# Kernel optimization log

Measured on AMD Instinct MI355X. Metric: run time of the kernel, lower is better.

Reference implementation:

```python
import jax, jax.numpy as jnp
import numpy as np

N_EMBD = 2048
N_HEAD = 16
N_HIDDEN = 5632  # find_multiple(int(2*4*2048/3), 256)
EPS = 1e-5
BETA = 1.0


def rmsnorm(x, scale):
    # mean of squares computed in fp32 as in the torch code
    norm = jnp.mean(x.astype(jnp.float32) ** 2, axis=-1, keepdims=True)
    x_normed = x * jax.lax.rsqrt(norm + EPS)
    return (scale * x_normed).astype(x.dtype)


def setup_inputs() -> dict:
    key = jax.random.key(0)
    ks = jax.random.split(key, 9)
    B, T, C = 1, 2048, N_EMBD
    s = lambda k, shape, fan: jax.random.normal(k, shape, jnp.float32) * (1.0 / np.sqrt(fan))
    return {
        "x": jax.random.normal(ks[0], (B, T, C), jnp.float32),
        "alibi": jax.random.normal(ks[1], (N_HEAD, T, T), jnp.float32),
        "w_attn": s(ks[2], (C, 3 * C), C),   # c_attn weight (in, out) layout
        "w_proj": s(ks[3], (C, C), C),
        "w_fc1": s(ks[4], (C, N_HIDDEN), C),
        "w_fc2": s(ks[5], (C, N_HIDDEN), C),
        "w_mlp_proj": s(ks[6], (N_HIDDEN, C), N_HIDDEN),
        "rms1_scale": jnp.ones((C,), jnp.float32),
        "rms2_scale": jnp.ones((C,), jnp.float32),
    }


def attention(x, alibi, w_attn, w_proj):
    B, T, C = x.shape
    hd = C // N_HEAD
    qkv = x @ w_attn  # [B,T,3C]
    q, k, v = jnp.split(qkv, 3, axis=-1)
    q = q.reshape(B, T, N_HEAD, hd).transpose(0, 2, 1, 3)  # [B,H,T,hd]
    k = k.reshape(B, T, N_HEAD, hd).transpose(0, 2, 1, 3)
    v = v.reshape(B, T, N_HEAD, hd).transpose(0, 2, 1, 3)
    scale = 1.0 / np.sqrt(hd)
    scores = jnp.einsum("bhqd,bhkd->bhqk", q, k) * scale + BETA * alibi  # [B,H,T,T]
    causal = jnp.tril(jnp.ones((T, T), bool))
    scores = jnp.where(causal, scores, -jnp.inf)
    attn = jax.nn.softmax(scores, axis=-1)
    y = jnp.einsum("bhqk,bhkd->bhqd", attn, v)
    y = y.transpose(0, 2, 1, 3).reshape(B, T, C)
    return y @ w_proj


def mlp(x, w_fc1, w_fc2, w_mlp_proj):
    return (jax.nn.silu(x @ w_fc1) * (x @ w_fc2)) @ w_mlp_proj


def reference(x, alibi, w_attn, w_proj, w_fc1, w_fc2, w_mlp_proj, rms1_scale, rms2_scale):
    x = x + attention(rmsnorm(x, rms1_scale), alibi, w_attn, w_proj)
    x = x + mlp(rmsnorm(x, rms2_scale), w_fc1, w_fc2, w_mlp_proj)
    return x
```

## Files before the change

kernel.cpp:

```cpp
#include <hip/hip_runtime.h>
#include <stdint.h>

typedef __attribute__((ext_vector_type(4))) float f32x4;
typedef __attribute__((ext_vector_type(8))) __bf16 bf8_t;
typedef __attribute__((ext_vector_type(8))) uint16_t u16x8;

typedef __attribute__((address_space(1))) uint8_t as1_u8;
typedef __attribute__((address_space(3))) uint8_t as3_u8;

__device__ inline void async_copy16(const void* g, void* l) {
  __builtin_amdgcn_global_load_lds((const as1_u8*)g, (as3_u8*)l, 16, 0, 0);
}

__device__ inline uint16_t f2bf(float f) {
  uint32_t u = __builtin_bit_cast(uint32_t, f);
  u = (u + 0x7fff + ((u >> 16) & 1)) >> 16;
  return (uint16_t)u;
}
__device__ inline float bf2f(uint16_t h) {
  uint32_t u = ((uint32_t)h) << 16;
  return __builtin_bit_cast(float, u);
}
__device__ inline int swz(int r) { return (((r & 7) ^ ((r >> 3) & 7)) << 4); }
__device__ inline int vswz(int r) { return ((r & 7) << 4); }

__global__ __launch_bounds__(256) void rmsnorm_kernel(const float* __restrict__ X,
                                                      const float* __restrict__ S,
                                                      uint16_t* __restrict__ O) {
  const int row = blockIdx.x;
  const int tid = threadIdx.x;
  const float* xr = X + (size_t)row * 2048;
  float4 v1 = ((const float4*)xr)[tid * 2];
  float4 v2 = ((const float4*)xr)[tid * 2 + 1];
  float ss = v1.x * v1.x + v1.y * v1.y + v1.z * v1.z + v1.w * v1.w +
             v2.x * v2.x + v2.y * v2.y + v2.z * v2.z + v2.w * v2.w;
  #pragma unroll
  for (int m = 1; m < 64; m <<= 1) ss += __shfl_xor(ss, m);
  __shared__ float wsum[4];
  if ((tid & 63) == 0) wsum[tid >> 6] = ss;
  __syncthreads();
  float tot = wsum[0] + wsum[1] + wsum[2] + wsum[3];
  float inv = rsqrtf(tot * (1.0f / 2048.0f) + 1e-5f);
  const int base = tid * 8;
  const float* sc = S + base;
  float xs[8] = {v1.x, v1.y, v1.z, v1.w, v2.x, v2.y, v2.z, v2.w};
  u16x8 o;
  #pragma unroll
  for (int j = 0; j < 8; j++) o[j] = f2bf(xs[j] * inv * sc[j]);
  *(u16x8*)(O + (size_t)row * 2048 + base) = o;
}

__global__ __launch_bounds__(256) void transpose_conv(const float* __restrict__ W,
                                                      uint16_t* __restrict__ WT,
                                                      int K, int N) {
  __shared__ float tile[64][65];
  const int n0 = blockIdx.x * 64, k0 = blockIdx.y * 64;
  const int tid = threadIdx.x;
  const int lr = tid >> 4;
  const int lc = (tid & 15) * 4;
  #pragma unroll
  for (int i = 0; i < 4; i++) {
    const float4 v = *(const float4*)&W[(size_t)(k0 + lr + i * 16) * N + n0 + lc];
    tile[lr + i * 16][lc] = v.x;
    tile[lr + i * 16][lc + 1] = v.y;
    tile[lr + i * 16][lc + 2] = v.z;
    tile[lr + i * 16][lc + 3] = v.w;
  }
  __syncthreads();
  const int tn = tid >> 3;
  const int tk = (tid & 7) * 8;
  #pragma unroll
  for (int i = 0; i < 2; i++) {
    u16x8 o;
    #pragma unroll
    for (int j = 0; j < 8; j++) o[j] = f2bf(tile[tk + j][tn + i * 32]);
    *(u16x8*)&WT[(size_t)(n0 + tn + i * 32) * K + k0 + tk] = o;
  }
}

__global__ __launch_bounds__(256) void transpose_v(const uint16_t* __restrict__ qkv,
                                                   uint16_t* __restrict__ vT) {
  __shared__ uint16_t tile[64][68];
  const int t0 = blockIdx.x * 64;
  const int c0 = blockIdx.y * 64;
  const int tid = threadIdx.x;
  const int lr = tid >> 3;
  const int lc = (tid & 7) * 8;
  #pragma unroll
  for (int i = 0; i < 2; i++) {
    const int r = lr + i * 32;
    u16x8 v = *(const u16x8*)&qkv[(size_t)(t0 + r) * 6144 + 4096 + c0 + lc];
    #pragma unroll
    for (int j = 0; j < 8; j++) tile[lc + j][r] = v[j];
  }
  __syncthreads();
  #pragma unroll
  for (int i = 0; i < 2; i++) {
    const int c = lr + i * 32;
    u16x8 o = *(const u16x8*)&tile[c][lc];
    *(u16x8*)&vT[(size_t)(c0 + c) * 2048 + t0 + lc] = o;
  }
}

enum { EPI_BF16 = 0, EPI_ADDF32 = 1, EPI_SILUMUL = 2 };

__device__ inline void gemm_epi(int EPI, void* Cout, const void* RES, size_t idx, float v) {
  if (EPI == EPI_BF16) {
    ((uint16_t*)Cout)[idx] = f2bf(v);
  } else if (EPI == EPI_ADDF32) {
    ((float*)Cout)[idx] = ((const float*)RES)[idx] + v;
  } else {
    const float g = bf2f(((const uint16_t*)RES)[idx]);
    const float sg = g / (1.0f + __expf(-g));
    ((uint16_t*)Cout)[idx] = f2bf(sg * v);
  }
}

template <int EPI>
__global__ __launch_bounds__(256, 2) void gemm_bt(const uint16_t* __restrict__ A,
                                                  const uint16_t* __restrict__ BT,
                                                  void* __restrict__ Cout,
                                                  const void* __restrict__ RES,
                                                  int M, int N, int K) {
  __shared__ uint16_t As[128 * 32];
  __shared__ uint16_t Bs[128 * 32];
  const int tid = threadIdx.x;
  const int lane = tid & 63;
  const int w = tid >> 6;
  const int l15 = lane & 15, l4 = lane >> 4;
  const int m0 = blockIdx.y * 128, n0 = blockIdx.x * 128;
  const int wr = w >> 1, wc = w & 1;

  f32x4 acc[4][4];
  #pragma unroll
  for (int i = 0; i < 4; i++)
    #pragma unroll
    for (int j = 0; j < 4; j++) acc[i][j] = 0.0f;

  for (int kk = 0; kk < K; kk += 32) {
    __syncthreads();
    #pragma unroll
    for (int s = 0; s < 2; s++) {
      const int bu = s * 256 + w * 64;
      const int unit = bu + lane;
      const int row = unit >> 2, ch = unit & 3;
      async_copy16(A + (size_t)(m0 + row) * K + kk + ch * 8, (char*)As + bu * 16);
      async_copy16(BT + (size_t)(n0 + row) * K + kk + ch * 8, (char*)Bs + bu * 16);
    }
    __syncthreads();
    bf8_t a[4], b[4];
    #pragma unroll
    for (int mi = 0; mi < 4; mi++)
      a[mi] = *(const bf8_t*)(As + (wr * 64 + mi * 16 + l15) * 32 + l4 * 8);
    #pragma unroll
    for (int ni = 0; ni < 4; ni++)
      b[ni] = *(const bf8_t*)(Bs + (wc * 64 + ni * 16 + l15) * 32 + l4 * 8);
    #pragma unroll
    for (int mi = 0; mi < 4; mi++)
      #pragma unroll
      for (int ni = 0; ni < 4; ni++)
        acc[mi][ni] = __builtin_amdgcn_mfma_f32_16x16x32_bf16(a[mi], b[ni], acc[mi][ni], 0, 0, 0);
  }

  #pragma unroll
  for (int mi = 0; mi < 4; mi++) {
    #pragma unroll
    for (int ni = 0; ni < 4; ni++) {
      #pragma unroll
      for (int r = 0; r < 4; r++) {
        const int row = m0 + wr * 64 + mi * 16 + l4 * 4 + r;
        const int col = n0 + wc * 64 + ni * 16 + l15;
        gemm_epi(EPI, Cout, RES, (size_t)row * N + col, acc[mi][ni][r]);
      }
    }
  }
}

template <int EPI>
__global__ __launch_bounds__(256, 3) void gemm_bt64(const uint16_t* __restrict__ A,
                                                    const uint16_t* __restrict__ BT,
                                                    void* __restrict__ Cout,
                                                    const void* __restrict__ RES,
                                                    int M, int N, int K) {
  __shared__ uint16_t As[128 * 32];
  __shared__ uint16_t Bs[64 * 32];
  const int tid = threadIdx.x;
  const int lane = tid & 63;
  const int w = tid >> 6;
  const int l15 = lane & 15, l4 = lane >> 4;
  const int m0 = blockIdx.y * 128, n0 = blockIdx.x * 64;

  f32x4 acc[2][4];
  #pragma unroll
  for (int i = 0; i < 2; i++)
    #pragma unroll
    for (int j = 0; j < 4; j++) acc[i][j] = 0.0f;

  for (int kk = 0; kk < K; kk += 32) {
    __syncthreads();
    #pragma unroll
    for (int s = 0; s < 2; s++) {
      const int bu = s * 256 + w * 64;
      const int unit = bu + lane;
      const int row = unit >> 2, ch = unit & 3;
      async_copy16(A + (size_t)(m0 + row) * K + kk + ch * 8, (char*)As + bu * 16);
    }
    {
      const int bu = w * 64;
      const int unit = bu + lane;
      const int row = unit >> 2, ch = unit & 3;
      async_copy16(BT + (size_t)(n0 + row) * K + kk + ch * 8, (char*)Bs + bu * 16);
    }
    __syncthreads();
    bf8_t a[2], b[4];
    #pragma unroll
    for (int mi = 0; mi < 2; mi++)
      a[mi] = *(const bf8_t*)(As + (w * 32 + mi * 16 + l15) * 32 + l4 * 8);
    #pragma unroll
    for (int ni = 0; ni < 4; ni++)
      b[ni] = *(const bf8_t*)(Bs + (ni * 16 + l15) * 32 + l4 * 8);
    #pragma unroll
    for (int mi = 0; mi < 2; mi++)
      #pragma unroll
      for (int ni = 0; ni < 4; ni++)
        acc[mi][ni] = __builtin_amdgcn_mfma_f32_16x16x32_bf16(a[mi], b[ni], acc[mi][ni], 0, 0, 0);
  }

  #pragma unroll
  for (int mi = 0; mi < 2; mi++) {
    #pragma unroll
    for (int ni = 0; ni < 4; ni++) {
      #pragma unroll
      for (int r = 0; r < 4; r++) {
        const int row = m0 + w * 32 + mi * 16 + l4 * 4 + r;
        const int col = n0 + ni * 16 + l15;
        gemm_epi(EPI, Cout, RES, (size_t)row * N + col, acc[mi][ni][r]);
      }
    }
  }
}

__global__ __launch_bounds__(256, 2) void attn_kernel(const uint16_t* __restrict__ qkv,
                                                      const uint16_t* __restrict__ vT,
                                                      const float* __restrict__ alibi,
                                                      uint16_t* __restrict__ Y) {
  const int h = blockIdx.y;
  const int qt = 31 - blockIdx.x;
  const int tid = threadIdx.x;
  const int lane = tid & 63;
  const int w = tid >> 6;
  const int l15 = lane & 15, l4 = lane >> 4;

  __shared__ uint16_t Ks[2][64 * 128];
  __shared__ uint16_t Vs[2][128 * 64];
  __shared__ uint16_t Ps[4][16 * 64];

  const float scale = 0.08838834764831845f;

  auto stage = [&](int kv0, int b) {
    #pragma unroll
    for (int i = 0; i < 4; i++) {
      const int u = tid + i * 256;
      const int r = u >> 4;
      const int c = (u & 15) ^ ((r & 7) ^ ((r >> 3) & 7));
      async_copy16(qkv + (size_t)(kv0 + r) * 6144 + 2048 + h * 128 + c * 8,
                   (char*)Ks[b] + u * 16);
    }
    #pragma unroll
    for (int i = 0; i < 4; i++) {
      const int u = tid + i * 256;
      const int r = u >> 3;
      const int c = (u & 7) ^ (r & 7);
      async_copy16(vT + (size_t)(h * 128 + r) * 2048 + kv0 + c * 8,
                   (char*)Vs[b] + u * 16);
    }
  };
  auto load_al = [&](int kv0, float (&al)[4][4]) {
    #pragma unroll
    for (int r = 0; r < 4; r++) {
      const size_t rowb = ((size_t)h * 2048 + (qt * 64 + w * 16 + l4 * 4 + r)) * 2048;
      #pragma unroll
      for (int nf = 0; nf < 4; nf++)
        al[nf][r] = alibi[rowb + kv0 + nf * 16 + l15];
    }
  };

  const int qrow = qt * 64 + w * 16 + l15;
  bf8_t qf[4];
  #pragma unroll
  for (int kc = 0; kc < 4; kc++)
    qf[kc] = *(const bf8_t*)(qkv + (size_t)qrow * 6144 + h * 128 + kc * 32 + l4 * 8);

  f32x4 accy[8];
  #pragma unroll
  for (int i = 0; i < 8; i++) accy[i] = 0.0f;
  float mrun[4], lrun[4];
  #pragma unroll
  for (int r = 0; r < 4; r++) { mrun[r] = -1e30f; lrun[r] = 0.0f; }

  stage(0, 0);
  float al[4][4];
  load_al(0, al);

  for (int kvt = 0; kvt <= qt; kvt++) {
    const int b = kvt & 1;
    const int kv0 = kvt * 64;
    __syncthreads();

    const int kvn = (kvt < qt) ? (kvt + 1) : qt;
    float aln[4][4];
    load_al(kvn * 64, aln);
    stage(kvn * 64, b ^ 1);

    float s[4][4];
    #pragma unroll
    for (int nf = 0; nf < 4; nf++) {
      f32x4 sa = 0.0f;
      const int krow = nf * 16 + l15;
      #pragma unroll
      for (int kc = 0; kc < 4; kc++) {
        bf8_t kb = *(const bf8_t*)((const char*)Ks[b] +
                                   ((krow * 256 + kc * 64 + l4 * 16) ^ swz(krow)));
        sa = __builtin_amdgcn_mfma_f32_16x16x32_bf16(qf[kc], kb, sa, 0, 0, 0);
      }
      const int kvcol = kv0 + nf * 16 + l15;
      #pragma unroll
      for (int r = 0; r < 4; r++) {
        const int q = qt * 64 + w * 16 + l4 * 4 + r;
        float sv = sa[r] * scale + al[nf][r];
        if (kvcol > q) sv = -1e30f;
        s[nf][r] = sv;
      }
    }

    #pragma unroll
    for (int r = 0; r < 4; r++) {
      float rm = fmaxf(fmaxf(s[0][r], s[1][r]), fmaxf(s[2][r], s[3][r]));
      rm = fmaxf(rm, __shfl_xor(rm, 1));
      rm = fmaxf(rm, __shfl_xor(rm, 2));
      rm = fmaxf(rm, __shfl_xor(rm, 4));
      rm = fmaxf(rm, __shfl_xor(rm, 8));
      const float mnew = fmaxf(mrun[r], rm);
      const float alpha = __expf(mrun[r] - mnew);
      mrun[r] = mnew;
      float rs = 0.0f;
      #pragma unroll
      for (int nf = 0; nf < 4; nf++) {
        const float p = __expf(s[nf][r] - mnew);
        s[nf][r] = p;
        rs += p;
      }
      rs += __shfl_xor(rs, 1);
      rs += __shfl_xor(rs, 2);
      rs += __shfl_xor(rs, 4);
      rs += __shfl_xor(rs, 8);
      lrun[r] = lrun[r] * alpha + rs;
      #pragma unroll
      for (int df = 0; df < 8; df++) accy[df][r] *= alpha;
    }

    #pragma unroll
    for (int nf = 0; nf < 4; nf++) {
      #pragma unroll
      for (int r = 0; r < 4; r++) {
        const int rq = l4 * 4 + r;
        const int bo = (rq * 128 + (nf * 16 + l15) * 2) ^ vswz(rq);
        *(uint16_t*)((char*)Ps[w] + bo) = f2bf(s[nf][r]);
      }
    }

    #pragma unroll
    for (int kk = 0; kk < 2; kk++) {
      bf8_t pa = *(const bf8_t*)((const char*)Ps[w] +
                                 ((l15 * 128 + kk * 64 + l4 * 16) ^ vswz(l15)));
      #pragma unroll
      for (int df = 0; df < 8; df++) {
        const int vr = df * 16 + l15;
        bf8_t vb = *(const bf8_t*)((const char*)Vs[b] +
                                   ((vr * 128 + kk * 64 + l4 * 16) ^ vswz(vr)));
        accy[df] = __builtin_amdgcn_mfma_f32_16x16x32_bf16(pa, vb, accy[df], 0, 0, 0);
      }
    }

    #pragma unroll
    for (int nf = 0; nf < 4; nf++)
      #pragma unroll
      for (int r = 0; r < 4; r++) al[nf][r] = aln[nf][r];
  }

  #pragma unroll
  for (int df = 0; df < 8; df++) {
    #pragma unroll
    for (int r = 0; r < 4; r++) {
      const int row = qt * 64 + w * 16 + l4 * 4 + r;
      const int col = h * 128 + df * 16 + l15;
      Y[(size_t)row * 2048 + col] = f2bf(accy[df][r] / lrun[r]);
    }
  }
}

extern "C" void kernel_launch(void* const* d_in, const int* in_sizes, int n_in,
                              void* d_out, int out_size, void* d_ws, size_t ws_size,
                              hipStream_t stream) {
  const float* x      = (const float*)d_in[0];
  const float* alibi  = (const float*)d_in[1];
  const float* w_attn = (const float*)d_in[2];
  const float* w_proj = (const float*)d_in[3];
  const float* w_fc1  = (const float*)d_in[4];
  const float* w_fc2  = (const float*)d_in[5];
  const float* w_mp   = (const float*)d_in[6];
  const float* rms1   = (const float*)d_in[7];
  const float* rms2   = (const float*)d_in[8];
  float* out = (float*)d_out;

  char* ws = (char*)d_ws;
  uint16_t* xn      = (uint16_t*)(ws + 0);
  uint16_t* qkv     = (uint16_t*)(ws + 8388608);
  uint16_t* y       = (uint16_t*)(ws + 33554432);
  uint16_t* g1      = (uint16_t*)(ws + 41943040);
  uint16_t* hbuf    = (uint16_t*)(ws + 65011712);
  uint16_t* wt_attn = (uint16_t*)(ws + 88080384);
  uint16_t* wt_proj = (uint16_t*)(ws + 113246208);
  uint16_t* wt_fc1  = (uint16_t*)(ws + 121634816);
  uint16_t* wt_fc2  = (uint16_t*)(ws + 144703488);
  uint16_t* wt_mp   = (uint16_t*)(ws + 167772160);
  uint16_t* vT      = (uint16_t*)(ws + 190840832);

  transpose_conv<<<dim3(6144 / 64, 2048 / 64), 256, 0, stream>>>(w_attn, wt_attn, 2048, 6144);
  transpose_conv<<<dim3(2048 / 64, 2048 / 64), 256, 0, stream>>>(w_proj, wt_proj, 2048, 2048);
  transpose_conv<<<dim3(5632 / 64, 2048 / 64), 256, 0, stream>>>(w_fc1, wt_fc1, 2048, 5632);
  transpose_conv<<<dim3(5632 / 64, 2048 / 64), 256, 0, stream>>>(w_fc2, wt_fc2, 2048, 5632);
  transpose_conv<<<dim3(2048 / 64, 5632 / 64), 256, 0, stream>>>(w_mp, wt_mp, 5632, 2048);

  rmsnorm_kernel<<<2048, 256, 0, stream>>>(x, rms1, xn);

  gemm_bt<EPI_BF16><<<dim3(6144 / 128, 2048 / 128), 256, 0, stream>>>(
      xn, wt_attn, qkv, nullptr, 2048, 6144, 2048);

  transpose_v<<<dim3(32, 32), 256, 0, stream>>>(qkv, vT);

  attn_kernel<<<dim3(32, 16), 256, 0, stream>>>(qkv, vT, alibi, y);

  gemm_bt64<EPI_ADDF32><<<dim3(2048 / 64, 2048 / 128), 256, 0, stream>>>(
      y, wt_proj, out, x, 2048, 2048, 2048);

  rmsnorm_kernel<<<2048, 256, 0, stream>>>(out, rms2, xn);

  gemm_bt<EPI_BF16><<<dim3(5632 / 128, 2048 / 128), 256, 0, stream>>>(
      xn, wt_fc1, g1, nullptr, 2048, 5632, 2048);

  gemm_bt<EPI_SILUMUL><<<dim3(5632 / 128, 2048 / 128), 256, 0, stream>>>(
      xn, wt_fc2, hbuf, g1, 2048, 5632, 2048);

  gemm_bt64<EPI_ADDF32><<<dim3(2048 / 64, 2048 / 128), 256, 0, stream>>>(
      hbuf, wt_mp, out, out, 2048, 2048, 5632);
}
```

Before: 563.9 us.

## Add 256x256-tile 8-wave pingpong GEMM for QKV and MLP up-projections

Introduces a new bf16 GEMM kernel with 256x256 output tiles, 512 threads (8 waves in a 2x4 grid) and double-buffered LDS. It streams K in half-tile pieces interleaved with MFMA quadrants, separated by barriers and raised wave priority during MFMA. It replaces the 128x128 gemm_bt for the QKV, fc1 and fc2 projections to raise per-block data reuse and overlap global loads with compute. The cost is 128 KB of LDS per block, heavy register use, and far fewer blocks: 192 for QKV and 176 for fc, close to the CU count, which risks wave-quantization and occupancy problems.

```diff
diff --git a/kernel.cpp b/kernel.cpp
--- a/kernel.cpp
+++ b/kernel.cpp
@@ -240,6 +240,153 @@
   }
 }
 
+template <int EPI>
+__global__ __launch_bounds__(512, 2) void gemm8p(const uint16_t* __restrict__ A,
+                                                 const uint16_t* __restrict__ BT,
+                                                 void* __restrict__ Cout,
+                                                 const void* __restrict__ RES,
+                                                 int M, int N, int K) {
+  __shared__ uint16_t Ald[2][256 * 64];
+  __shared__ uint16_t Bld[2][256 * 64];
+  const int tid = threadIdx.x;
+  const int lane = tid & 63;
+  const int w = tid >> 6;
+  const int l15 = lane & 15, l4 = lane >> 4;
+  const int wm = w >> 2, wn = w & 3;
+  const int m0 = blockIdx.y * 256, n0 = blockIdx.x * 256;
+
+  f32x4 acc[8][4];
+  #pragma unroll
+  for (int i = 0; i < 8; i++)
+    #pragma unroll
+    for (int j = 0; j < 4; j++) acc[i][j] = 0.0f;
+
+  auto stageHalf = [&](const uint16_t* G, int row0, int kt, char* ldsBase) {
+    #pragma unroll
+    for (int i = 0; i < 2; i++) {
+      const int u = i * 512 + w * 64 + lane;
+      const int r = u >> 3;
+      const int c = (u & 7) ^ (r & 7);
+      async_copy16(G + (size_t)(row0 + r) * K + kt + c * 8,
+                   ldsBase + (i * 512 + w * 64) * 16);
+    }
+  };
+
+  bf8_t aF[8], bF[4];
+  auto ldsA = [&](int b, int mh) {
+    const char* base = (const char*)&Ald[b][0];
+    #pragma unroll
+    for (int mi = 0; mi < 4; mi++)
+      #pragma unroll
+      for (int ks = 0; ks < 2; ks++) {
+        const int R = wm * 128 + mh * 64 + mi * 16 + l15;
+        aF[mi * 2 + ks] = *(const bf8_t*)(base + R * 128 + (((ks * 4 + l4) ^ (R & 7)) * 16));
+      }
+  };
+  auto ldsB = [&](int b, int nh) {
+    const char* base = (const char*)&Bld[b][0];
+    #pragma unroll
+    for (int ni = 0; ni < 2; ni++)
+      #pragma unroll
+      for (int ks = 0; ks < 2; ks++) {
+        const int R = wn * 64 + nh * 32 + ni * 16 + l15;
+        bF[ni * 2 + ks] = *(const bf8_t*)(base + R * 128 + (((ks * 4 + l4) ^ (R & 7)) * 16));
+      }
+  };
+  auto mfmaQ = [&](int mh, int nh) {
+    __builtin_amdgcn_s_setprio(1);
+    #pragma unroll
+    for (int mi = 0; mi < 4; mi++)
+      #pragma unroll
+      for (int ni = 0; ni < 2; ni++)
+        #pragma unroll
+        for (int ks = 0; ks < 2; ks++)
+          acc[mh * 4 + mi][nh * 2 + ni] = __builtin_amdgcn_mfma_f32_16x16x32_bf16(
+              aF[mi * 2 + ks], bF[ni * 2 + ks], acc[mh * 4 + mi][nh * 2 + ni], 0, 0, 0);
+    __builtin_amdgcn_s_setprio(0);
+  };
+
+  stageHalf(A, m0, 0, (char*)&Ald[0][0]);
+  stageHalf(A, m0 + 128, 0, (char*)&Ald[0][0] + 16384);
+  stageHalf(BT, n0, 0, (char*)&Bld[0][0]);
+  stageHalf(BT, n0 + 128, 0, (char*)&Bld[0][0] + 16384);
+  stageHalf(A, m0, 64, (char*)&Ald[1][0]);
+  asm volatile("s_waitcnt vmcnt(2)" ::: "memory");
+  __builtin_amdgcn_s_barrier();
+
+  const int NT = K >> 6;
+  const int NJ = NT >> 1;
+  for (int j = 0; j < NJ; ++j) {
+    const int t1k = (2 * j + 1) << 6;
+    const int t2k = (2 * j + 2) << 6;
+    const int t3k = (2 * j + 3) << 6;
+    const bool more = (j + 1 < NJ);
+
+    ldsA(0, 0); ldsB(0, 0);
+    stageHalf(A, m0 + 128, t1k, (char*)&Ald[1][0] + 16384);
+    __builtin_amdgcn_s_barrier();
+    mfmaQ(0, 0);
+    __builtin_amdgcn_s_barrier();
+    ldsB(0, 1);
+    stageHalf(BT, n0, t1k, (char*)&Bld[1][0]);
+    __builtin_amdgcn_s_barrier();
+    mfmaQ(0, 1);
+    __builtin_amdgcn_s_barrier();
+    ldsA(0, 1);
+    stageHalf(BT, n0 + 128, t1k, (char*)&Bld[1][0] + 16384);
+    __builtin_amdgcn_s_barrier();
+    mfmaQ(1, 1);
+    __builtin_amdgcn_s_barrier();
+    ldsB(0, 0);
+    if (more) {
+      stageHalf(A, m0, t2k, (char*)&Ald[0][0]);
+      asm volatile("s_waitcnt vmcnt(2)" ::: "memory");
+    } else {
+      asm volatile("s_waitcnt vmcnt(0)" ::: "memory");
+    }
+    __builtin_amdgcn_s_barrier();
+    mfmaQ(1, 0);
+    __builtin_amdgcn_s_barrier();
+    ldsA(1, 0); ldsB(1, 0);
+    if (more) stageHalf(A, m0 + 128, t2k, (char*)&Ald[0][0] + 16384);
+    __builtin_amdgcn_s_barrier();
+    mfmaQ(0, 0);
+    __builtin_amdgcn_s_barrier();
+    ldsB(1, 1);
+    if (more) stageHalf(BT, n0, t2k, (char*)&Bld[0][0]);
+    __builtin_amdgcn_s_barrier();
+    mfmaQ(0, 1);
+    __builtin_amdgcn_s_barrier();
+    ldsA(1, 1);
+    if (more) stageHalf(BT, n0 + 128, t2k, (char*)&Bld[0][0] + 16384);
+    __builtin_amdgcn_s_barrier();
+    mfmaQ(1, 1);
+    __builtin_amdgcn_s_barrier();
+    ldsB(1, 0);
+    if (more) {
+      stageHalf(A, m0, t3k, (char*)&Ald[1][0]);
+      asm volatile("s_waitcnt vmcnt(2)" ::: "memory");
+    } else {
+      asm volatile("s_waitcnt vmcnt(0)" ::: "memory");
+    }
+    __builtin_amdgcn_s_barrier();
+    mfmaQ(1, 0);
+    __builtin_amdgcn_s_barrier();
+  }
+
+  #pragma unroll
+  for (int ai = 0; ai < 8; ai++) {
+    #pragma unroll
+    for (int bj = 0; bj < 4; bj++) {
+      const int row0 = m0 + wm * 128 + (ai >> 2) * 64 + (ai & 3) * 16 + l4 * 4;
+      const int col = n0 + wn * 64 + (bj >> 1) * 32 + (bj & 1) * 16 + l15;
+      #pragma unroll
+      for (int r = 0; r < 4; r++)
+        gemm_epi(EPI, Cout, RES, (size_t)(row0 + r) * N + col, acc[ai][bj][r]);
+    }
+  }
+}
+
 __global__ __launch_bounds__(256, 2) void attn_kernel(const uint16_t* __restrict__ qkv,
                                                       const uint16_t* __restrict__ vT,
                                                       const float* __restrict__ alibi,
@@ -434,7 +581,7 @@
 
   rmsnorm_kernel<<<2048, 256, 0, stream>>>(x, rms1, xn);
 
-  gemm_bt<EPI_BF16><<<dim3(6144 / 128, 2048 / 128), 256, 0, stream>>>(
+  gemm8p<EPI_BF16><<<dim3(6144 / 256, 2048 / 256), 512, 0, stream>>>(
       xn, wt_attn, qkv, nullptr, 2048, 6144, 2048);
 
   transpose_v<<<dim3(32, 32), 256, 0, stream>>>(qkv, vT);
@@ -446,10 +593,10 @@
 
   rmsnorm_kernel<<<2048, 256, 0, stream>>>(out, rms2, xn);
 
-  gemm_bt<EPI_BF16><<<dim3(5632 / 128, 2048 / 128), 256, 0, stream>>>(
+  gemm8p<EPI_BF16><<<dim3(5632 / 256, 2048 / 256), 512, 0, stream>>>(
       xn, wt_fc1, g1, nullptr, 2048, 5632, 2048);
 
-  gemm_bt<EPI_SILUMUL><<<dim3(5632 / 128, 2048 / 128), 256, 0, stream>>>(
+  gemm8p<EPI_SILUMUL><<<dim3(5632 / 256, 2048 / 256), 512, 0, stream>>>(
       xn, wt_fc2, hbuf, g1, 2048, 5632, 2048);
 
   gemm_bt64<EPI_ADDF32><<<dim3(2048 / 64, 2048 / 128), 256, 0, stream>>>(
```

New measurement: 602.3 us. 6.8% more time.

## Split attention KV range across blocks with merge pass, fuse weight transposes

Applied to the files above, without the earlier changes.

Attention now splits each (head, query-tile) KV loop across up to four blocks, writing unnormalized partial accumulators with running max and sum, then merges them in a separate kernel. This addresses the causal load imbalance and low block count (512 blocks) of the original attention kernel. The five weight-transpose launches are combined into one kernel, and s_setprio hints are added around the MFMA sections. The cost is extra fp32 partial traffic to global memory, one more launch, and a final merge pass.

```diff
diff --git a/kernel.cpp b/kernel.cpp
--- a/kernel.cpp
+++ b/kernel.cpp
@@ -50,12 +50,10 @@
   *(u16x8*)(O + (size_t)row * 2048 + base) = o;
 }
 
-__global__ __launch_bounds__(256) void transpose_conv(const float* __restrict__ W,
-                                                      uint16_t* __restrict__ WT,
-                                                      int K, int N) {
+__device__ inline void transpose_tile(const float* __restrict__ W, uint16_t* __restrict__ WT,
+                                      int K, int N, int bx, int by, int tid) {
   __shared__ float tile[64][65];
-  const int n0 = blockIdx.x * 64, k0 = blockIdx.y * 64;
-  const int tid = threadIdx.x;
+  const int n0 = bx * 64, k0 = by * 64;
   const int lr = tid >> 4;
   const int lc = (tid & 15) * 4;
   #pragma unroll
@@ -75,6 +73,32 @@
     #pragma unroll
     for (int j = 0; j < 8; j++) o[j] = f2bf(tile[tk + j][tn + i * 32]);
     *(u16x8*)&WT[(size_t)(n0 + tn + i * 32) * K + k0 + tk] = o;
+  }
+}
+
+__global__ __launch_bounds__(256) void transpose_all(
+    const float* __restrict__ w_attn, const float* __restrict__ w_proj,
+    const float* __restrict__ w_fc1, const float* __restrict__ w_fc2,
+    const float* __restrict__ w_mp,
+    uint16_t* __restrict__ wt_attn, uint16_t* __restrict__ wt_proj,
+    uint16_t* __restrict__ wt_fc1, uint16_t* __restrict__ wt_fc2,
+    uint16_t* __restrict__ wt_mp) {
+  int idx = blockIdx.x;
+  const int tid = threadIdx.x;
+  if (idx < 3072) {
+    transpose_tile(w_attn, wt_attn, 2048, 6144, idx % 96, idx / 96, tid);
+  } else if (idx < 4096) {
+    idx -= 3072;
+    transpose_tile(w_proj, wt_proj, 2048, 2048, idx % 32, idx / 32, tid);
+  } else if (idx < 6912) {
+    idx -= 4096;
+    transpose_tile(w_fc1, wt_fc1, 2048, 5632, idx % 88, idx / 88, tid);
+  } else if (idx < 9728) {
+    idx -= 6912;
+    transpose_tile(w_fc2, wt_fc2, 2048, 5632, idx % 88, idx / 88, tid);
+  } else {
+    idx -= 9728;
+    transpose_tile(w_mp, wt_mp, 5632, 2048, idx % 32, idx / 32, tid);
   }
 }
 
@@ -240,12 +264,19 @@
   }
 }
 
-__global__ __launch_bounds__(256, 2) void attn_kernel(const uint16_t* __restrict__ qkv,
-                                                      const uint16_t* __restrict__ vT,
-                                                      const float* __restrict__ alibi,
-                                                      uint16_t* __restrict__ Y) {
-  const int h = blockIdx.y;
-  const int qt = 31 - blockIdx.x;
+#define PART_STRIDE (64 * 128 + 128)
+__global__ __launch_bounds__(256, 2) void attn_part(const uint16_t* __restrict__ qkv,
+                                                    const uint16_t* __restrict__ vT,
+                                                    const float* __restrict__ alibi,
+                                                    float* __restrict__ part) {
+  const int p = blockIdx.x;
+  const int qt = 31 - blockIdx.y;
+  const int h = blockIdx.z;
+  const int c = (qt + 4) >> 2;
+  const int start = p * c;
+  const int end = min((p + 1) * c, qt + 1);
+  if (start >= end) return;
+
   const int tid = threadIdx.x;
   const int lane = tid & 63;
   const int w = tid >> 6;
@@ -262,16 +293,16 @@
     for (int i = 0; i < 4; i++) {
       const int u = tid + i * 256;
       const int r = u >> 4;
-      const int c = (u & 15) ^ ((r & 7) ^ ((r >> 3) & 7));
-      async_copy16(qkv + (size_t)(kv0 + r) * 6144 + 2048 + h * 128 + c * 8,
+      const int cc = (u & 15) ^ ((r & 7) ^ ((r >> 3) & 7));
+      async_copy16(qkv + (size_t)(kv0 + r) * 6144 + 2048 + h * 128 + cc * 8,
                    (char*)Ks[b] + u * 16);
     }
     #pragma unroll
     for (int i = 0; i < 4; i++) {
       const int u = tid + i * 256;
       const int r = u >> 3;
-      const int c = (u & 7) ^ (r & 7);
-      async_copy16(vT + (size_t)(h * 128 + r) * 2048 + kv0 + c * 8,
+      const int cc = (u & 7) ^ (r & 7);
+      async_copy16(vT + (size_t)(h * 128 + r) * 2048 + kv0 + cc * 8,
                    (char*)Vs[b] + u * 16);
     }
   };
@@ -298,16 +329,16 @@
   #pragma unroll
   for (int r = 0; r < 4; r++) { mrun[r] = -1e30f; lrun[r] = 0.0f; }
 
-  stage(0, 0);
+  stage(start * 64, 0);
   float al[4][4];
-  load_al(0, al);
-
-  for (int kvt = 0; kvt <= qt; kvt++) {
-    const int b = kvt & 1;
+  load_al(start * 64, al);
+
+  for (int kvt = start; kvt < end; kvt++) {
+    const int b = (kvt - start) & 1;
     const int kv0 = kvt * 64;
     __syncthreads();
 
-    const int kvn = (kvt < qt) ? (kvt + 1) : qt;
+    const int kvn = (kvt + 1 < end) ? (kvt + 1) : kvt;
     float aln[4][4];
     load_al(kvn * 64, aln);
     stage(kvn * 64, b ^ 1);
@@ -317,12 +348,14 @@
     for (int nf = 0; nf < 4; nf++) {
       f32x4 sa = 0.0f;
       const int krow = nf * 16 + l15;
+      __builtin_amdgcn_s_setprio(1);
       #pragma unroll
       for (int kc = 0; kc < 4; kc++) {
         bf8_t kb = *(const bf8_t*)((const char*)Ks[b] +
                                    ((krow * 256 + kc * 64 + l4 * 16) ^ swz(krow)));
         sa = __builtin_amdgcn_mfma_f32_16x16x32_bf16(qf[kc], kb, sa, 0, 0, 0);
       }
+      __builtin_amdgcn_s_setprio(0);
       const int kvcol = kv0 + nf * 16 + l15;
       #pragma unroll
       for (int r = 0; r < 4; r++) {
@@ -346,9 +379,9 @@
       float rs = 0.0f;
       #pragma unroll
       for (int nf = 0; nf < 4; nf++) {
-        const float p = __expf(s[nf][r] - mnew);
-        s[nf][r] = p;
-        rs += p;
+        const float pp = __expf(s[nf][r] - mnew);
+        s[nf][r] = pp;
+        rs += pp;
       }
       rs += __shfl_xor(rs, 1);
       rs += __shfl_xor(rs, 2);
@@ -369,6 +402,7 @@
       }
     }
 
+    __builtin_amdgcn_s_setprio(1);
     #pragma unroll
     for (int kk = 0; kk < 2; kk++) {
       bf8_t pa = *(const bf8_t*)((const char*)Ps[w] +
@@ -381,6 +415,7 @@
         accy[df] = __builtin_amdgcn_mfma_f32_16x16x32_bf16(pa, vb, accy[df], 0, 0, 0);
       }
     }
+    __builtin_amdgcn_s_setprio(0);
 
     #pragma unroll
     for (int nf = 0; nf < 4; nf++)
@@ -388,14 +423,63 @@
       for (int r = 0; r < 4; r++) al[nf][r] = aln[nf][r];
   }
 
+  float* pb = part + (size_t)(((h * 32 + qt) * 4) + p) * PART_STRIDE;
   #pragma unroll
   for (int df = 0; df < 8; df++) {
     #pragma unroll
     for (int r = 0; r < 4; r++) {
-      const int row = qt * 64 + w * 16 + l4 * 4 + r;
-      const int col = h * 128 + df * 16 + l15;
-      Y[(size_t)row * 2048 + col] = f2bf(accy[df][r] / lrun[r]);
-    }
+      const int row = w * 16 + l4 * 4 + r;
+      pb[row * 128 + df * 16 + l15] = accy[df][r];
+    }
+  }
+  if (l15 == 0) {
+    #pragma unroll
+    for (int r = 0; r < 4; r++) {
+      const int row = w * 16 + l4 * 4 + r;
+      pb[8192 + row] = mrun[r];
+      pb[8192 + 64 + row] = lrun[r];
+    }
+  }
+}
+
+__global__ __launch_bounds__(256) void attn_merge(const float* __restrict__ part,
+                                                  uint16_t* __restrict__ Y) {
+  const int qt = blockIdx.x;
+  const int h = blockIdx.y;
+  const int c = (qt + 4) >> 2;
+  const int cnt = (qt + c) / c;
+  const int tid = threadIdx.x;
+  const int row = tid >> 2;
+  const int cg = (tid & 3) * 32;
+
+  const float* pb = part + (size_t)((h * 32 + qt) * 4) * PART_STRIDE;
+
+  float m_p[4], w_p[4];
+  float M = -1e30f;
+  for (int p = 0; p < cnt; p++) {
+    m_p[p] = pb[p * PART_STRIDE + 8192 + row];
+    M = fmaxf(M, m_p[p]);
+  }
+  float L = 0.0f;
+  for (int p = 0; p < cnt; p++) {
+    w_p[p] = __expf(m_p[p] - M);
+    L += w_p[p] * pb[p * PART_STRIDE + 8192 + 64 + row];
+  }
+  const float invL = 1.0f / L;
+
+  uint16_t* yr = Y + (size_t)(qt * 64 + row) * 2048 + h * 128 + cg;
+  #pragma unroll
+  for (int j = 0; j < 32; j += 8) {
+    f32x4 s0 = 0.0f, s1 = 0.0f;
+    for (int p = 0; p < cnt; p++) {
+      const float* ap = pb + p * PART_STRIDE + row * 128 + cg + j;
+      s0 += w_p[p] * *(const f32x4*)ap;
+      s1 += w_p[p] * *(const f32x4*)(ap + 4);
+    }
+    u16x8 o;
+    #pragma unroll
+    for (int e = 0; e < 4; e++) { o[e] = f2bf(s0[e] * invL); o[e + 4] = f2bf(s1[e] * invL); }
+    *(u16x8*)(yr + j) = o;
   }
 }
 
@@ -425,12 +509,10 @@
   uint16_t* wt_fc2  = (uint16_t*)(ws + 144703488);
   uint16_t* wt_mp   = (uint16_t*)(ws + 167772160);
   uint16_t* vT      = (uint16_t*)(ws + 190840832);
-
-  transpose_conv<<<dim3(6144 / 64, 2048 / 64), 256, 0, stream>>>(w_attn, wt_attn, 2048, 6144);
-  transpose_conv<<<dim3(2048 / 64, 2048 / 64), 256, 0, stream>>>(w_proj, wt_proj, 2048, 2048);
-  transpose_conv<<<dim3(5632 / 64, 2048 / 64), 256, 0, stream>>>(w_fc1, wt_fc1, 2048, 5632);
-  transpose_conv<<<dim3(5632 / 64, 2048 / 64), 256, 0, stream>>>(w_fc2, wt_fc2, 2048, 5632);
-  transpose_conv<<<dim3(2048 / 64, 5632 / 64), 256, 0, stream>>>(w_mp, wt_mp, 5632, 2048);
+  float*    part    = (float*)(ws + 199229440);
+
+  transpose_all<<<12544, 256, 0, stream>>>(w_attn, w_proj, w_fc1, w_fc2, w_mp,
+                                           wt_attn, wt_proj, wt_fc1, wt_fc2, wt_mp);
 
   rmsnorm_kernel<<<2048, 256, 0, stream>>>(x, rms1, xn);
 
@@ -439,7 +521,9 @@
 
   transpose_v<<<dim3(32, 32), 256, 0, stream>>>(qkv, vT);
 
-  attn_kernel<<<dim3(32, 16), 256, 0, stream>>>(qkv, vT, alibi, y);
+  attn_part<<<dim3(4, 32, 16), 256, 0, stream>>>(qkv, vT, alibi, part);
+
+  attn_merge<<<dim3(32, 16), 256, 0, stream>>>(part, y);
 
   gemm_bt64<EPI_ADDF32><<<dim3(2048 / 64, 2048 / 128), 256, 0, stream>>>(
       y, wt_proj, out, x, 2048, 2048, 2048);
```

After: 562.5 us. No clear change (-0.2%).
